# Kernel optimization log

Measured on AMD Instinct MI355X. Metric: run time of the kernel, lower is better.

## Reference

```python
import jax, jax.numpy as jnp
import numpy as np

T, B, E, H = 1000, 8, 1024, 16
HD = E // H


def _rope(x):
    # x: (B*H, T, HD); matches RotaryEmbedding.encode_pos (seq_dim=1)
    t = jnp.arange(x.shape[1], dtype=jnp.float32)
    inv_freq = 1.0 / (10000.0 ** (jnp.arange(0, HD, 2, dtype=jnp.float32) / HD))
    freqs = t[:, None] * inv_freq[None, :]            # (T, HD/2)
    emb = jnp.concatenate([freqs, freqs], axis=-1)    # (T, HD)
    cos, sin = jnp.cos(emb)[None], jnp.sin(emb)[None]  # (1, T, HD)
    x1, x2 = jnp.split(x, 2, axis=-1)
    rot = jnp.concatenate([-x2, x1], axis=-1)
    return cos * x + sin * rot


def setup_inputs() -> dict:
    key = jax.random.key(0)
    ks = jax.random.split(key, 8)
    d = {
        'query': jax.random.normal(ks[0], (T, B, E), jnp.float32),
        'key':   jax.random.normal(ks[1], (T, B, E), jnp.float32),
        'value': jax.random.normal(ks[2], (T, B, E), jnp.float32),
        'q_w': jax.random.normal(ks[3], (E, E), jnp.float32) * 0.02,
        'k_w': jax.random.normal(ks[4], (E, E), jnp.float32) * 0.02,
        'v_w': jax.random.normal(ks[5], (E, E), jnp.float32) * 0.02,
        'o_w': jax.random.normal(ks[6], (E, E), jnp.float32) * 0.02,
        'q_b': jnp.zeros((E,), jnp.float32),
        'k_b': jnp.zeros((E,), jnp.float32),
        'v_b': jnp.zeros((E,), jnp.float32),
        'o_b': jnp.zeros((E,), jnp.float32),
    }
    return d


def reference(query, key, value, q_w, q_b, k_w, k_b, v_w, v_b, o_w, o_b):
    tgt_len, bsz, embed_dim = query.shape
    scaling = HD ** -0.5
    # nn.Linear: x @ W^T + b
    q = (query @ q_w.T + q_b) * scaling
    k = key @ k_w.T + k_b
    v = value @ v_w.T + v_b
    # (T, B, E) -> (B*H, T, HD)
    def split_heads(x):
        return x.reshape(tgt_len, bsz * H, HD).transpose(1, 0, 2)
    q, k, v = split_heads(q), split_heads(k), split_heads(v)
    q, k = _rope(q), _rope(k)
    attn_weights = jnp.einsum('bqd,bkd->bqk', q, k)              # (B*H, T, T)
    attn_probs = jax.nn.softmax(attn_weights.astype(jnp.float32), axis=-1).astype(attn_weights.dtype)
    attn = jnp.einsum('bqk,bkd->bqd', attn_probs, v)             # (B*H, T, HD)
    attn = attn.transpose(1, 0, 2).reshape(tgt_len, bsz, embed_dim)
    out = attn @ o_w.T + o_b
    return out
```

## Files before the change

### kernel.cpp

```cpp
#include <hip/hip_runtime.h>
#include <hip/hip_bf16.h>

#define T_DIM 1000
#define B_DIM 8
#define E_DIM 1024
#define H_DIM 16
#define HD_DIM 64
#define M_DIM 8000
#define BH_DIM 128

typedef float f4 __attribute__((ext_vector_type(4)));
typedef float f16v __attribute__((ext_vector_type(16)));
typedef __bf16 b8 __attribute__((ext_vector_type(8)));
typedef unsigned long long u64;

__device__ __forceinline__ short f2bf(float f) {
  unsigned u = __float_as_uint(f);
  u = u + 0x7fffu + ((u >> 16) & 1u);
  return (short)(u >> 16);
}

__device__ __forceinline__ unsigned cvt_pk_bf16(float lo, float hi) {
  unsigned r;
  asm("v_cvt_pk_bf16_f32 %0, %1, %2" : "=v"(r) : "v"(lo), "v"(hi));
  return r;
}

__device__ __forceinline__ void gload_lds16(const void* g, void* l) {
  __builtin_amdgcn_global_load_lds(
      (const __attribute__((address_space(1))) void*)g,
      (__attribute__((address_space(3))) void*)l, 16, 0, 0);
}

__device__ __forceinline__ void cvt_quad(const float* src, short* dst) {
  float4 v = *(const float4*)src;
  short4 o;
  o.x = f2bf(v.x); o.y = f2bf(v.y); o.z = f2bf(v.z); o.w = f2bf(v.w);
  *(short4*)dst = o;
}

__global__ void convert_w(const float* __restrict__ a, const float* __restrict__ b,
                          const float* __restrict__ c, const float* __restrict__ d,
                          short* __restrict__ dst) {
  const int nq = (4 * 1048576) / 4;
  for (int i = blockIdx.x * blockDim.x + threadIdx.x; i < nq; i += gridDim.x * blockDim.x) {
    int mat = i >> 18;
    int w = (i & 262143) * 4;
    const float* src = mat == 0 ? a : (mat == 1 ? b : (mat == 2 ? c : d));
    cvt_quad(src + w, dst + i * 4);
  }
}

__global__ void convert_x(const float* __restrict__ src, short* __restrict__ dst) {
  const int nq = (M_DIM * E_DIM) / 4;
  for (int i = blockIdx.x * blockDim.x + threadIdx.x; i < nq; i += gridDim.x * blockDim.x) {
    cvt_quad(src + i * 4, dst + i * 4);
  }
}

__global__ void prep_all(const float* __restrict__ qw, const float* __restrict__ kw,
                         const float* __restrict__ vw, const float* __restrict__ ow,
                         const float* __restrict__ xq, const float* __restrict__ xk,
                         const float* __restrict__ xv,
                         short* __restrict__ wbf, short* __restrict__ xqb,
                         short* __restrict__ xkb, short* __restrict__ xvb) {
  const int WQ = 1048576;
  const int XQ = (M_DIM * E_DIM) / 4;
  const int total = WQ + 3 * XQ;
  for (int i = blockIdx.x * blockDim.x + threadIdx.x; i < total; i += gridDim.x * blockDim.x) {
    if (i < WQ) {
      int mat = i >> 18;
      int w = (i & 262143) * 4;
      const float* src = mat == 0 ? qw : (mat == 1 ? kw : (mat == 2 ? vw : ow));
      cvt_quad(src + w, wbf + i * 4);
    } else {
      int j = i - WQ;
      if (j < XQ) cvt_quad(xq + j * 4, xqb + j * 4);
      else if (j < 2 * XQ) cvt_quad(xk + (j - XQ) * 4, xkb + (j - XQ) * 4);
      else cvt_quad(xv + (j - 2 * XQ) * 4, xvb + (j - 2 * XQ) * 4);
    }
  }
}

__global__ void rope_tab(float* __restrict__ cosd, float* __restrict__ sind) {
  int i = blockIdx.x * blockDim.x + threadIdx.x;
  if (i >= T_DIM * 32) return;
  int t = i >> 5, f = i & 31;
  double inv = pow(10000.0, -(double)f / 32.0);
  double a = (double)t * inv;
  cosd[i] = (float)cos(a);
  sind[i] = (float)sin(a);
}

__global__ __launch_bounds__(256, 2) void proj_gemm(
    const short* __restrict__ xqb, const short* __restrict__ xkb,
    const short* __restrict__ xvb, const short* __restrict__ wbf_all,
    const float* __restrict__ qb, const float* __restrict__ kb,
    const float* __restrict__ vb,
    short* __restrict__ qpk, short* __restrict__ kpk, short* __restrict__ vtp,
    const float* __restrict__ ropec, const float* __restrict__ ropes, int mode_base) {
  int mode = mode_base + blockIdx.y;
  const short* xbf = mode == 0 ? xqb : (mode == 1 ? xkb : xvb);
  const short* W = wbf_all + mode * 1048576;
  const float* bias = mode == 0 ? qb : (mode == 1 ? kb : vb);

  int id = blockIdx.x;
  int w = (id & 7) * 63 + (id >> 3);
  int n0 = (w & 7) * 128;
  int m0 = (w >> 3) * 128;
  __shared__ short As[2][128 * 64];
  __shared__ short Bs[2][128 * 64];
  int tid = threadIdx.x;
  int l = tid & 63, wid = tid >> 6;
  int wr = wid >> 1, wc = wid & 1;
  int lane16 = l & 15, lgrp = l >> 4;

  f4 acc[4][4];
#pragma unroll
  for (int i = 0; i < 4; ++i)
#pragma unroll
    for (int j = 0; j < 4; ++j)
#pragma unroll
      for (int r = 0; r < 4; ++r) acc[i][j][r] = 0.f;

  auto stage = [&](int kt, int buf) {
    int k0 = kt * 64;
#pragma unroll
    for (int j = 0; j < 4; ++j) {
      int idx = tid + j * 256;
      int r = idx >> 3, s = idx & 7;
      int c = s ^ (r & 7);
      int gm = m0 + r; gm = gm < M_DIM ? gm : (M_DIM - 1);
      gload_lds16(xbf + gm * 1024 + k0 + c * 8, &As[buf][idx * 8]);
      gload_lds16(W + (n0 + r) * 1024 + k0 + c * 8, &Bs[buf][idx * 8]);
    }
  };

  stage(0, 0);
  __syncthreads();

  for (int kt = 0; kt < 16; ++kt) {
    int b = kt & 1;
    if (kt < 15) stage(kt + 1, b ^ 1);
    b8 af[2][4], bf[2][4];
#pragma unroll
    for (int kk = 0; kk < 2; ++kk) {
#pragma unroll
      for (int mf = 0; mf < 4; ++mf) {
        int row = wr * 64 + mf * 16 + lane16;
        af[kk][mf] = *(const b8*)(&As[b][0] + row * 64 + ((((kk << 2) + lgrp) ^ (row & 7)) << 3));
      }
#pragma unroll
      for (int nf = 0; nf < 4; ++nf) {
        int row = wc * 64 + nf * 16 + lane16;
        bf[kk][nf] = *(const b8*)(&Bs[b][0] + row * 64 + ((((kk << 2) + lgrp) ^ (row & 7)) << 3));
      }
    }
    __builtin_amdgcn_s_setprio(1);
#pragma unroll
    for (int kk = 0; kk < 2; ++kk)
#pragma unroll
      for (int mf = 0; mf < 4; ++mf)
#pragma unroll
        for (int nf = 0; nf < 4; ++nf)
          acc[mf][nf] = __builtin_amdgcn_mfma_f32_16x16x32_bf16(af[kk][mf], bf[kk][nf], acc[mf][nf], 0, 0, 0);
    __builtin_amdgcn_s_setprio(0);
    __syncthreads();
  }

  int h = (n0 + wc * 64) >> 6;
  float bv[4];
#pragma unroll
  for (int nf = 0; nf < 4; ++nf) bv[nf] = bias[n0 + wc * 64 + nf * 16 + lane16];
  const float qs = 0.125f * 1.44269504088896f;

#pragma unroll
  for (int mf = 0; mf < 4; ++mf) {
#pragma unroll
    for (int r = 0; r < 4; ++r) {
      int gm = m0 + wr * 64 + mf * 16 + lgrp * 4 + r;
      bool valid = gm < M_DIM;
      int t = gm >> 3, bb = gm & 7;
      int tc = t < T_DIM ? t : (T_DIM - 1);
      float x0 = acc[mf][0][r] + bv[0];
      float x1 = acc[mf][1][r] + bv[1];
      float x2 = acc[mf][2][r] + bv[2];
      float x3 = acc[mf][3][r] + bv[3];
      if (mode == 0) { x0 *= qs; x1 *= qs; x2 *= qs; x3 *= qs; }
      if (mode < 2) {
        float c0 = ropec[tc * 32 + lane16],      s0 = ropes[tc * 32 + lane16];
        float c1 = ropec[tc * 32 + 16 + lane16], s1 = ropes[tc * 32 + 16 + lane16];
        float y0 = c0 * x0 - s0 * x2;
        float y2 = c0 * x2 + s0 * x0;
        float y1 = c1 * x1 - s1 * x3;
        float y3 = c1 * x3 + s1 * x1;
        if (valid) {
          short* dst = (mode == 0 ? qpk : kpk) + (bb * 16 + h) * 64000 + t * 64;
          dst[lane16]      = f2bf(y0);
          dst[16 + lane16] = f2bf(y1);
          dst[32 + lane16] = f2bf(y2);
          dst[48 + lane16] = f2bf(y3);
        }
      } else if (valid) {
        short* dst = vtp + (bb * 16 + h) * 64000 + t;
        dst[(lane16) * 1000]      = f2bf(x0);
        dst[(16 + lane16) * 1000] = f2bf(x1);
        dst[(32 + lane16) * 1000] = f2bf(x2);
        dst[(48 + lane16) * 1000] = f2bf(x3);
      }
    }
  }
}

__global__ __launch_bounds__(256, 4) void attn_fused(
    const short* __restrict__ qpk, const short* __restrict__ kpk,
    const short* __restrict__ vtp, short* __restrict__ apk) {
  int id = blockIdx.x;
  int xcd = id & 7, seq = id >> 3;
  int bh = xcd * 16 + (seq >> 3);
  int q0 = (seq & 7) * 128;
  int tid = threadIdx.x;
  int l = tid & 63, wid = tid >> 6;
  int l31 = l & 31, hi = l >> 5, l7 = l & 7;
  int qg = q0 + wid * 32 + l31;

  __shared__ short Ks[2][64 * 64];
  __shared__ short Vs[2][64 * 64];

  const short* qh = qpk + bh * 64000;
  const short* kh = kpk + bh * 64000;
  const short* vh = vtp + bh * 64000;

  int srow = tid >> 3;
  int sslot = tid & 7;

  b8 bq[4];
  {
    int t = qg < T_DIM ? qg : (T_DIM - 1);
#pragma unroll
    for (int hc = 0; hc < 4; ++hc)
      bq[hc] = *(const b8*)(qh + t * 64 + hc * 16 + hi * 8);
  }

  float lrun = 0.f;
  f16v o0, o1;
#pragma unroll
  for (int i = 0; i < 16; ++i) { o0[i] = 0.f; o1[i] = 0.f; }

  auto stageK = [&](int st, int buf) {
    int s0 = st * 64;
#pragma unroll
    for (int j = 0; j < 2; ++j) {
      int r = srow + j * 32;
      int c = sslot ^ (r & 7);
      gload_lds16(kh + (s0 + r) * 64 + c * 8, &Ks[buf][(j * 256 + tid) * 8]);
    }
  };
  auto stageV = [&](int st, int buf) {
    int s0 = st * 64;
#pragma unroll
    for (int j = 0; j < 2; ++j) {
      int r = srow + j * 32;
      int c = sslot ^ (r & 7);
      gload_lds16(vh + r * 1000 + s0 + c * 8, &Vs[buf][(j * 256 + tid) * 8]);
    }
  };

  stageK(0, 0);
  stageV(0, 0);
  stageK(1, 1);
  __syncthreads();

  f16v c0v, c1v;
#pragma unroll
  for (int i = 0; i < 16; ++i) { c0v[i] = 0.f; c1v[i] = 0.f; }
#pragma unroll
  for (int hc = 0; hc < 4; ++hc) {
    int slot = ((2 * hc + hi) ^ l7) << 3;
    b8 a0 = *(const b8*)(Ks[0] + l31 * 64 + slot);
    b8 a1 = *(const b8*)(Ks[0] + (32 + l31) * 64 + slot);
    c0v = __builtin_amdgcn_mfma_f32_32x32x16_bf16(a0, bq[hc], c0v, 0, 0, 0);
    c1v = __builtin_amdgcn_mfma_f32_32x32x16_bf16(a1, bq[hc], c1v, 0, 0, 0);
  }
  __syncthreads();

  for (int i = 0; i < 16; ++i) {
    int b = i & 1;
    if (i < 14) stageK(i + 2, b);
    if (i < 15) stageV(i + 1, b ^ 1);

    if (i == 15) {
#pragma unroll
      for (int r = 4; r < 16; ++r) c1v[r] = -1e30f;
    }

#pragma unroll
    for (int j = 0; j < 16; ++j) {
      c0v[j] = __builtin_amdgcn_exp2f(c0v[j]);
      c1v[j] = __builtin_amdgcn_exp2f(c1v[j]);
    }
    float ts[8];
#pragma unroll
    for (int j = 0; j < 8; ++j) ts[j] = (c0v[j] + c0v[j + 8]) + (c1v[j] + c1v[j + 8]);
#pragma unroll
    for (int d = 4; d > 0; d >>= 1)
#pragma unroll
      for (int j = 0; j < d; ++j) ts[j] += ts[j + d];
    lrun += ts[0];

    unsigned u0[8], u1[8];
#pragma unroll
    for (int j = 0; j < 8; ++j) {
      u0[j] = cvt_pk_bf16(c0v[2 * j], c0v[2 * j + 1]);
      u1[j] = cvt_pk_bf16(c1v[2 * j], c1v[2 * j + 1]);
    }
    union { unsigned u[4]; b8 v; } pf[4];
    {
      auto w0 = __builtin_amdgcn_permlane32_swap(u0[0], u0[2], false, false);
      auto w1 = __builtin_amdgcn_permlane32_swap(u0[1], u0[3], false, false);
      pf[0].u[0] = w0[0]; pf[0].u[1] = w1[0]; pf[0].u[2] = w0[1]; pf[0].u[3] = w1[1];
      auto w2 = __builtin_amdgcn_permlane32_swap(u0[4], u0[6], false, false);
      auto w3 = __builtin_amdgcn_permlane32_swap(u0[5], u0[7], false, false);
      pf[1].u[0] = w2[0]; pf[1].u[1] = w3[0]; pf[1].u[2] = w2[1]; pf[1].u[3] = w3[1];
      auto w4 = __builtin_amdgcn_permlane32_swap(u1[0], u1[2], false, false);
      auto w5 = __builtin_amdgcn_permlane32_swap(u1[1], u1[3], false, false);
      pf[2].u[0] = w4[0]; pf[2].u[1] = w5[0]; pf[2].u[2] = w4[1]; pf[2].u[3] = w5[1];
      auto w6 = __builtin_amdgcn_permlane32_swap(u1[4], u1[6], false, false);
      auto w7 = __builtin_amdgcn_permlane32_swap(u1[5], u1[7], false, false);
      pf[3].u[0] = w6[0]; pf[3].u[1] = w7[0]; pf[3].u[2] = w6[1]; pf[3].u[3] = w7[1];
    }

    if (i < 15) {
      const short* Kb = Ks[b ^ 1];
#pragma unroll
      for (int j = 0; j < 16; ++j) { c0v[j] = 0.f; c1v[j] = 0.f; }
      __builtin_amdgcn_s_setprio(1);
#pragma unroll
      for (int hc = 0; hc < 4; ++hc) {
        int slot = ((2 * hc + hi) ^ l7) << 3;
        b8 a0 = *(const b8*)(Kb + l31 * 64 + slot);
        b8 a1 = *(const b8*)(Kb + (32 + l31) * 64 + slot);
        c0v = __builtin_amdgcn_mfma_f32_32x32x16_bf16(a0, bq[hc], c0v, 0, 0, 0);
        c1v = __builtin_amdgcn_mfma_f32_32x32x16_bf16(a1, bq[hc], c1v, 0, 0, 0);
      }
      __builtin_amdgcn_s_setprio(0);
    }

    {
      const short* Vb = Vs[b];
      __builtin_amdgcn_s_setprio(1);
#pragma unroll
      for (int ck = 0; ck < 4; ++ck) {
        int slot = ((2 * ck + hi) ^ l7) << 3;
        b8 av0 = *(const b8*)(Vb + l31 * 64 + slot);
        b8 av1 = *(const b8*)(Vb + (32 + l31) * 64 + slot);
        o0 = __builtin_amdgcn_mfma_f32_32x32x16_bf16(av0, pf[ck].v, o0, 0, 0, 0);
        o1 = __builtin_amdgcn_mfma_f32_32x32x16_bf16(av1, pf[ck].v, o1, 0, 0, 0);
      }
      __builtin_amdgcn_s_setprio(0);
    }
    __syncthreads();
  }

  lrun += __shfl_xor(lrun, 32, 64);
  if (qg < T_DIM) {
    float linv = 1.f / lrun;
    int bb = bh >> 4, hh = bh & 15;
    short* dst = apk + (qg * 8 + bb) * 1024 + hh * 64;
#pragma unroll
    for (int rq = 0; rq < 4; ++rq) {
      int d0 = 8 * rq + 4 * hi;
      short4 w0, w1;
      w0.x = f2bf(o0[rq * 4 + 0] * linv);
      w0.y = f2bf(o0[rq * 4 + 1] * linv);
      w0.z = f2bf(o0[rq * 4 + 2] * linv);
      w0.w = f2bf(o0[rq * 4 + 3] * linv);
      w1.x = f2bf(o1[rq * 4 + 0] * linv);
      w1.y = f2bf(o1[rq * 4 + 1] * linv);
      w1.z = f2bf(o1[rq * 4 + 2] * linv);
      w1.w = f2bf(o1[rq * 4 + 3] * linv);
      *(short4*)(dst + d0) = w0;
      *(short4*)(dst + 32 + d0) = w1;
    }
  }
}

__global__ __launch_bounds__(256, 2) void out_gemm(
    const short* __restrict__ apk, const short* __restrict__ wo,
    const float* __restrict__ ob, float* __restrict__ out) {
  int id = blockIdx.x;
  int w = (id & 7) * 63 + (id >> 3);
  int n0 = (w & 7) * 128;
  int m0 = (w >> 3) * 128;
  __shared__ short As[2][128 * 64];
  __shared__ short Bs[2][128 * 64];
  int tid = threadIdx.x;
  int l = tid & 63, wid = tid >> 6;
  int wr = wid >> 1, wc = wid & 1;
  int lane16 = l & 15, lgrp = l >> 4;

  f4 acc[4][4];
#pragma unroll
  for (int i = 0; i < 4; ++i)
#pragma unroll
    for (int j = 0; j < 4; ++j)
#pragma unroll
      for (int r = 0; r < 4; ++r) acc[i][j][r] = 0.f;

  auto stage = [&](int kt, int buf) {
    int k0 = kt * 64;
#pragma unroll
    for (int j = 0; j < 4; ++j) {
      int idx = tid + j * 256;
      int r = idx >> 3, s = idx & 7;
      int c = s ^ (r & 7);
      int gm = m0 + r; gm = gm < M_DIM ? gm : (M_DIM - 1);
      gload_lds16(apk + gm * 1024 + k0 + c * 8, &As[buf][idx * 8]);
      gload_lds16(wo + (n0 + r) * 1024 + k0 + c * 8, &Bs[buf][idx * 8]);
    }
  };

  stage(0, 0);
  __syncthreads();

  for (int kt = 0; kt < 16; ++kt) {
    int b = kt & 1;
    if (kt < 15) stage(kt + 1, b ^ 1);
    b8 af[2][4], bf[2][4];
#pragma unroll
    for (int kk = 0; kk < 2; ++kk) {
#pragma unroll
      for (int mf = 0; mf < 4; ++mf) {
        int row = wr * 64 + mf * 16 + lane16;
        af[kk][mf] = *(const b8*)(&As[b][0] + row * 64 + ((((kk << 2) + lgrp) ^ (row & 7)) << 3));
      }
#pragma unroll
      for (int nf = 0; nf < 4; ++nf) {
        int row = wc * 64 + nf * 16 + lane16;
        bf[kk][nf] = *(const b8*)(&Bs[b][0] + row * 64 + ((((kk << 2) + lgrp) ^ (row & 7)) << 3));
      }
    }
    __builtin_amdgcn_s_setprio(1);
#pragma unroll
    for (int kk = 0; kk < 2; ++kk)
#pragma unroll
      for (int mf = 0; mf < 4; ++mf)
#pragma unroll
        for (int nf = 0; nf < 4; ++nf)
          acc[mf][nf] = __builtin_amdgcn_mfma_f32_16x16x32_bf16(af[kk][mf], bf[kk][nf], acc[mf][nf], 0, 0, 0);
    __builtin_amdgcn_s_setprio(0);
    __syncthreads();
  }

  float bv[4];
#pragma unroll
  for (int nf = 0; nf < 4; ++nf) bv[nf] = ob[n0 + wc * 64 + nf * 16 + lane16];
#pragma unroll
  for (int mf = 0; mf < 4; ++mf) {
#pragma unroll
    for (int r = 0; r < 4; ++r) {
      int gm = m0 + wr * 64 + mf * 16 + lgrp * 4 + r;
      if (gm < M_DIM) {
#pragma unroll
        for (int nf = 0; nf < 4; ++nf)
          out[gm * 1024 + n0 + wc * 64 + nf * 16 + lane16] = acc[mf][nf][r] + bv[nf];
      }
    }
  }
}

extern "C" void kernel_launch(void* const* d_in, const int* in_sizes, int n_in,
                              void* d_out, int out_size, void* d_ws, size_t ws_size,
                              hipStream_t stream) {
  const float* xq = (const float*)d_in[0];
  const float* xk = (const float*)d_in[1];
  const float* xv = (const float*)d_in[2];
  const float* qw = (const float*)d_in[3];
  const float* kw = (const float*)d_in[4];
  const float* vw = (const float*)d_in[5];
  const float* ow = (const float*)d_in[6];
  const float* qb = (const float*)d_in[7];
  const float* kb = (const float*)d_in[8];
  const float* vb = (const float*)d_in[9];
  const float* ob = (const float*)d_in[10];
  float* out = (float*)d_out;
  char* ws = (char*)d_ws;

  short* wbf   = (short*)(ws);
  float* ropec = (float*)(ws + 8388608);
  float* ropes = (float*)(ws + 8516608);
  short* qpk   = (short*)(ws + 8644608);
  short* kpk   = (short*)(ws + 8644608 + 16384512);
  short* vtp   = (short*)(ws + 8644608 + 2 * 16384512);
  short* apk   = (short*)(ws + 8644608 + 3 * 16384512);
  const size_t BASE = 8644608 + (size_t)4 * 16384512;

  hipMemsetAsync((char*)vtp + 2 * 8192000, 0, 512, stream);

  rope_tab<<<125, 256, 0, stream>>>(ropec, ropes);

  const size_t XB = (size_t)M_DIM * E_DIM * 2;
  if (ws_size >= BASE + 3 * XB) {
    short* xqb = (short*)(ws + BASE);
    short* xkb = (short*)(ws + BASE + XB);
    short* xvb = (short*)(ws + BASE + 2 * XB);
    prep_all<<<2048, 256, 0, stream>>>(qw, kw, vw, ow, xq, xk, xv, wbf, xqb, xkb, xvb);
    proj_gemm<<<dim3(504, 3), dim3(256), 0, stream>>>(xqb, xkb, xvb, wbf, qb, kb, vb,
                                                      qpk, kpk, vtp, ropec, ropes, 0);
  } else {
    short* xbf = apk;
    convert_w<<<2048, 256, 0, stream>>>(qw, kw, vw, ow, wbf);
    const float* xs[3] = {xq, xk, xv};
    for (int mode = 0; mode < 3; ++mode) {
      convert_x<<<2048, 256, 0, stream>>>(xs[mode], xbf);
      proj_gemm<<<dim3(504, 1), dim3(256), 0, stream>>>(xbf, xbf, xbf, wbf, qb, kb, vb,
                                                        qpk, kpk, vtp, ropec, ropes, mode);
    }
  }
  attn_fused<<<dim3(1024), dim3(256), 0, stream>>>(qpk, kpk, vtp, apk);
  out_gemm<<<dim3(504), dim3(256), 0, stream>>>(apk, wbf + 3 * 1048576, ob, out);
}
```

Measured before the change: 191.4 us.

## Halve GEMM K-tile to 32 and fold rope table and pad memset into prep

Both projection and output GEMMs now stage K in 32-wide tiles (32 iterations instead of 16) with a 4-chunk XOR swizzle, halving LDS per block so more blocks can be resident per CU. Separately, the rope table computation and the V padding zero-fill are merged into the prep_all conversion kernel, which removes a memset and a kernel launch on the main path. The smaller K-tile doubles the number of barriers and gives less work per stage to hide load latency.

```diff
diff --git a/kernel.cpp b/kernel.cpp
--- a/kernel.cpp
+++ b/kernel.cpp
@@ -63,21 +63,33 @@
                          const float* __restrict__ xq, const float* __restrict__ xk,
                          const float* __restrict__ xv,
                          short* __restrict__ wbf, short* __restrict__ xqb,
-                         short* __restrict__ xkb, short* __restrict__ xvb) {
+                         short* __restrict__ xkb, short* __restrict__ xvb,
+                         short* __restrict__ vtp_pad,
+                         float* __restrict__ ropec, float* __restrict__ ropes) {
   const int WQ = 1048576;
   const int XQ = (M_DIM * E_DIM) / 4;
-  const int total = WQ + 3 * XQ;
+  const int RP = T_DIM * 32;
+  const int total = WQ + 3 * XQ + RP + 256;
   for (int i = blockIdx.x * blockDim.x + threadIdx.x; i < total; i += gridDim.x * blockDim.x) {
     if (i < WQ) {
       int mat = i >> 18;
       int w = (i & 262143) * 4;
       const float* src = mat == 0 ? qw : (mat == 1 ? kw : (mat == 2 ? vw : ow));
       cvt_quad(src + w, wbf + i * 4);
-    } else {
+    } else if (i < WQ + 3 * XQ) {
       int j = i - WQ;
       if (j < XQ) cvt_quad(xq + j * 4, xqb + j * 4);
       else if (j < 2 * XQ) cvt_quad(xk + (j - XQ) * 4, xkb + (j - XQ) * 4);
       else cvt_quad(xv + (j - 2 * XQ) * 4, xvb + (j - 2 * XQ) * 4);
+    } else if (i < WQ + 3 * XQ + RP) {
+      int j = i - WQ - 3 * XQ;
+      int t = j >> 5, f = j & 31;
+      double inv = pow(10000.0, -(double)f / 32.0);
+      double a = (double)t * inv;
+      ropec[j] = (float)cos(a);
+      ropes[j] = (float)sin(a);
+    } else {
+      vtp_pad[i - WQ - 3 * XQ - RP] = 0;
     }
   }
 }
@@ -108,8 +120,8 @@
   int w = (id & 7) * 63 + (id >> 3);
   int n0 = (w & 7) * 128;
   int m0 = (w >> 3) * 128;
-  __shared__ short As[2][128 * 64];
-  __shared__ short Bs[2][128 * 64];
+  __shared__ short As[2][128 * 32];
+  __shared__ short Bs[2][128 * 32];
   int tid = threadIdx.x;
   int l = tid & 63, wid = tid >> 6;
   int wr = wid >> 1, wc = wid & 1;
@@ -124,12 +136,12 @@
       for (int r = 0; r < 4; ++r) acc[i][j][r] = 0.f;
 
   auto stage = [&](int kt, int buf) {
-    int k0 = kt * 64;
-#pragma unroll
-    for (int j = 0; j < 4; ++j) {
+    int k0 = kt * 32;
+#pragma unroll
+    for (int j = 0; j < 2; ++j) {
       int idx = tid + j * 256;
-      int r = idx >> 3, s = idx & 7;
-      int c = s ^ (r & 7);
+      int r = idx >> 2, s = idx & 3;
+      int c = s ^ ((r >> 1) & 3);
       int gm = m0 + r; gm = gm < M_DIM ? gm : (M_DIM - 1);
       gload_lds16(xbf + gm * 1024 + k0 + c * 8, &As[buf][idx * 8]);
       gload_lds16(W + (n0 + r) * 1024 + k0 + c * 8, &Bs[buf][idx * 8]);
@@ -139,31 +151,26 @@
   stage(0, 0);
   __syncthreads();
 
-  for (int kt = 0; kt < 16; ++kt) {
+  for (int kt = 0; kt < 32; ++kt) {
     int b = kt & 1;
-    if (kt < 15) stage(kt + 1, b ^ 1);
-    b8 af[2][4], bf[2][4];
-#pragma unroll
-    for (int kk = 0; kk < 2; ++kk) {
-#pragma unroll
-      for (int mf = 0; mf < 4; ++mf) {
-        int row = wr * 64 + mf * 16 + lane16;
-        af[kk][mf] = *(const b8*)(&As[b][0] + row * 64 + ((((kk << 2) + lgrp) ^ (row & 7)) << 3));
-      }
-#pragma unroll
-      for (int nf = 0; nf < 4; ++nf) {
-        int row = wc * 64 + nf * 16 + lane16;
-        bf[kk][nf] = *(const b8*)(&Bs[b][0] + row * 64 + ((((kk << 2) + lgrp) ^ (row & 7)) << 3));
-      }
+    if (kt < 31) stage(kt + 1, b ^ 1);
+    b8 af[4], bf[4];
+#pragma unroll
+    for (int mf = 0; mf < 4; ++mf) {
+      int row = wr * 64 + mf * 16 + lane16;
+      af[mf] = *(const b8*)(&As[b][0] + row * 32 + ((lgrp ^ ((row >> 1) & 3)) << 3));
+    }
+#pragma unroll
+    for (int nf = 0; nf < 4; ++nf) {
+      int row = wc * 64 + nf * 16 + lane16;
+      bf[nf] = *(const b8*)(&Bs[b][0] + row * 32 + ((lgrp ^ ((row >> 1) & 3)) << 3));
     }
     __builtin_amdgcn_s_setprio(1);
 #pragma unroll
-    for (int kk = 0; kk < 2; ++kk)
-#pragma unroll
-      for (int mf = 0; mf < 4; ++mf)
-#pragma unroll
-        for (int nf = 0; nf < 4; ++nf)
-          acc[mf][nf] = __builtin_amdgcn_mfma_f32_16x16x32_bf16(af[kk][mf], bf[kk][nf], acc[mf][nf], 0, 0, 0);
+    for (int mf = 0; mf < 4; ++mf)
+#pragma unroll
+      for (int nf = 0; nf < 4; ++nf)
+        acc[mf][nf] = __builtin_amdgcn_mfma_f32_16x16x32_bf16(af[mf], bf[nf], acc[mf][nf], 0, 0, 0);
     __builtin_amdgcn_s_setprio(0);
     __syncthreads();
   }
@@ -392,8 +399,8 @@
   int w = (id & 7) * 63 + (id >> 3);
   int n0 = (w & 7) * 128;
   int m0 = (w >> 3) * 128;
-  __shared__ short As[2][128 * 64];
-  __shared__ short Bs[2][128 * 64];
+  __shared__ short As[2][128 * 32];
+  __shared__ short Bs[2][128 * 32];
   int tid = threadIdx.x;
   int l = tid & 63, wid = tid >> 6;
   int wr = wid >> 1, wc = wid & 1;
@@ -408,12 +415,12 @@
       for (int r = 0; r < 4; ++r) acc[i][j][r] = 0.f;
 
   auto stage = [&](int kt, int buf) {
-    int k0 = kt * 64;
-#pragma unroll
-    for (int j = 0; j < 4; ++j) {
+    int k0 = kt * 32;
+#pragma unroll
+    for (int j = 0; j < 2; ++j) {
       int idx = tid + j * 256;
-      int r = idx >> 3, s = idx & 7;
-      int c = s ^ (r & 7);
+      int r = idx >> 2, s = idx & 3;
+      int c = s ^ ((r >> 1) & 3);
       int gm = m0 + r; gm = gm < M_DIM ? gm : (M_DIM - 1);
       gload_lds16(apk + gm * 1024 + k0 + c * 8, &As[buf][idx * 8]);
       gload_lds16(wo + (n0 + r) * 1024 + k0 + c * 8, &Bs[buf][idx * 8]);
@@ -423,31 +430,26 @@
   stage(0, 0);
   __syncthreads();
 
-  for (int kt = 0; kt < 16; ++kt) {
+  for (int kt = 0; kt < 32; ++kt) {
     int b = kt & 1;
-    if (kt < 15) stage(kt + 1, b ^ 1);
-    b8 af[2][4], bf[2][4];
-#pragma unroll
-    for (int kk = 0; kk < 2; ++kk) {
-#pragma unroll
-      for (int mf = 0; mf < 4; ++mf) {
-        int row = wr * 64 + mf * 16 + lane16;
-        af[kk][mf] = *(const b8*)(&As[b][0] + row * 64 + ((((kk << 2) + lgrp) ^ (row & 7)) << 3));
-      }
-#pragma unroll
-      for (int nf = 0; nf < 4; ++nf) {
-        int row = wc * 64 + nf * 16 + lane16;
-        bf[kk][nf] = *(const b8*)(&Bs[b][0] + row * 64 + ((((kk << 2) + lgrp) ^ (row & 7)) << 3));
-      }
+    if (kt < 31) stage(kt + 1, b ^ 1);
+    b8 af[4], bf[4];
+#pragma unroll
+    for (int mf = 0; mf < 4; ++mf) {
+      int row = wr * 64 + mf * 16 + lane16;
+      af[mf] = *(const b8*)(&As[b][0] + row * 32 + ((lgrp ^ ((row >> 1) & 3)) << 3));
+    }
+#pragma unroll
+    for (int nf = 0; nf < 4; ++nf) {
+      int row = wc * 64 + nf * 16 + lane16;
+      bf[nf] = *(const b8*)(&Bs[b][0] + row * 32 + ((lgrp ^ ((row >> 1) & 3)) << 3));
     }
     __builtin_amdgcn_s_setprio(1);
 #pragma unroll
-    for (int kk = 0; kk < 2; ++kk)
-#pragma unroll
-      for (int mf = 0; mf < 4; ++mf)
-#pragma unroll
-        for (int nf = 0; nf < 4; ++nf)
-          acc[mf][nf] = __builtin_amdgcn_mfma_f32_16x16x32_bf16(af[kk][mf], bf[kk][nf], acc[mf][nf], 0, 0, 0);
+    for (int mf = 0; mf < 4; ++mf)
+#pragma unroll
+      for (int nf = 0; nf < 4; ++nf)
+        acc[mf][nf] = __builtin_amdgcn_mfma_f32_16x16x32_bf16(af[mf], bf[nf], acc[mf][nf], 0, 0, 0);
     __builtin_amdgcn_s_setprio(0);
     __syncthreads();
   }
@@ -495,19 +497,18 @@
   short* apk   = (short*)(ws + 8644608 + 3 * 16384512);
   const size_t BASE = 8644608 + (size_t)4 * 16384512;
 
-  hipMemsetAsync((char*)vtp + 2 * 8192000, 0, 512, stream);
-
-  rope_tab<<<125, 256, 0, stream>>>(ropec, ropes);
-
   const size_t XB = (size_t)M_DIM * E_DIM * 2;
   if (ws_size >= BASE + 3 * XB) {
     short* xqb = (short*)(ws + BASE);
     short* xkb = (short*)(ws + BASE + XB);
     short* xvb = (short*)(ws + BASE + 2 * XB);
-    prep_all<<<2048, 256, 0, stream>>>(qw, kw, vw, ow, xq, xk, xv, wbf, xqb, xkb, xvb);
+    prep_all<<<2048, 256, 0, stream>>>(qw, kw, vw, ow, xq, xk, xv, wbf, xqb, xkb, xvb,
+                                       vtp + 8192000, ropec, ropes);
     proj_gemm<<<dim3(504, 3), dim3(256), 0, stream>>>(xqb, xkb, xvb, wbf, qb, kb, vb,
                                                       qpk, kpk, vtp, ropec, ropes, 0);
   } else {
+    hipMemsetAsync((char*)vtp + 2 * 8192000, 0, 512, stream);
+    rope_tab<<<125, 256, 0, stream>>>(ropec, ropes);
     short* xbf = apk;
     convert_w<<<2048, 256, 0, stream>>>(qw, kw, vw, ow, wbf);
     const float* xs[3] = {xq, xk, xv};
```

Measured after the change: 189.2 us. Within noise of the previous version (-1.2%).
